# Optimization experiments

Measured on AMD Instinct MI355X. Metric: run time of the kernel, lower is better.

## Reference

```python
import jax, jax.numpy as jnp
import numpy as np

GAMMA = 1.0
EPS = 1e-8


def setup_inputs() -> dict:
    key = jax.random.key(0)
    k1, k2 = jax.random.split(key)
    inputs = jax.random.normal(k1, (16, 2048, 1024), dtype=jnp.float32)
    codebook = jax.random.normal(k2, (2048, 1024), dtype=jnp.float32)  # normal(1.0) init
    return {"inputs": inputs, "codebook": codebook}


def reference(inputs, codebook):
    # inputs: [B, T, D]; codebook: [K, D]
    features = jax.lax.stop_gradient(inputs)
    # similarity = sum over D of features[..., None, :] * codebook -> [B, T, K]
    similarity = jnp.einsum('btd,kd->btk', features, codebook)
    scores = jax.nn.softmax(similarity, axis=-1)  # [B, T, K]
    nn_idx = jnp.argmax(scores, axis=-1)  # [B, T]
    # one_hot(nn_idx) @ codebook == direct gather
    quantized = codebook[nn_idx]  # [B, T, D]
    quantized = quantized - jnp.mean(quantized, axis=-1, keepdims=True)
    quantized = quantized / jnp.linalg.norm(quantized, axis=-1, keepdims=True)
    # entropy loss
    flat = scores.reshape(-1, scores.shape[-1])  # [B*T, K]
    h_clust = -jnp.mean(jnp.sum(flat * jnp.log2(flat + EPS), axis=-1))
    diversity = jnp.mean(flat, axis=0)  # [K]
    h_diversity = -jnp.sum(diversity * jnp.log2(diversity + EPS))
    loss = h_clust - GAMMA * h_diversity
    quantization_loss = jnp.full(scores.shape, loss)  # [B, T, K], scalar broadcast
    # straight-through estimator
    quantized = inputs + jax.lax.stop_gradient(quantized - inputs)
    return (quantized, quantization_loss, nn_idx, codebook)
```

## Files before the change

### kernel.cpp

```cpp
#include <hip/hip_runtime.h>
#include <math.h>

#define M_TOTAL 32768
#define D_DIM   1024
#define K_DIM   2048

#define OUT0_OFF 0ULL
#define OUT1_OFF 33554432ULL
#define OUT2_OFF 100663296ULL
#define OUT3_OFF 100696064ULL

typedef _Float16 f16x4 __attribute__((ext_vector_type(4)));
typedef _Float16 f16x8 __attribute__((ext_vector_type(8)));
typedef float    f32x4 __attribute__((ext_vector_type(4)));

__device__ __forceinline__ void async_copy16(void* lds, const void* g) {
    __builtin_amdgcn_global_load_lds(
        (const __attribute__((address_space(1))) unsigned int*)g,
        (__attribute__((address_space(3))) unsigned int*)lds, 16, 0, 0);
}

__global__ __launch_bounds__(256) void convcb_kernel(const float* __restrict__ C,
                                                     _Float16* __restrict__ ch,
                                                     _Float16* __restrict__ cl) {
    const int i = blockIdx.x * 256 + threadIdx.x;
    const float4 c = ((const float4*)C)[i];
    f16x4 h, l;
    h.x = (_Float16)c.x; l.x = (_Float16)(c.x - (float)h.x);
    h.y = (_Float16)c.y; l.y = (_Float16)(c.y - (float)h.y);
    h.z = (_Float16)c.z; l.z = (_Float16)(c.z - (float)h.z);
    h.w = (_Float16)c.w; l.w = (_Float16)(c.w - (float)h.w);
    ((f16x4*)ch)[i] = h;
    ((f16x4*)cl)[i] = l;
}

__global__ __launch_bounds__(256) void gemm_kernel(const float* __restrict__ X,
                                                   const _Float16* __restrict__ CH,
                                                   const _Float16* __restrict__ CL,
                                                   float* __restrict__ S) {
    __shared__ _Float16 Ah[128 * 32];
    __shared__ _Float16 Bh[128 * 32];
    __shared__ _Float16 Bl[128 * 32];

    const int tid  = threadIdx.x;
    const int lane = tid & 63;
    const int wave = tid >> 6;
    const int n0 = blockIdx.x * 128;
    const int m0 = blockIdx.y * 128;
    const int wm = (wave & 1) * 64;
    const int wn = (wave >> 1) * 64;
    const int fr = lane & 15;
    const int fq = lane >> 4;

    f32x4 acc[4][4];
#pragma unroll
    for (int mi = 0; mi < 4; mi++)
#pragma unroll
        for (int ni = 0; ni < 4; ni++) {
            acc[mi][ni].x = 0.f; acc[mi][ni].y = 0.f;
            acc[mi][ni].z = 0.f; acc[mi][ni].w = 0.f;
        }

    for (int k0 = 0; k0 < D_DIM; k0 += 32) {
#pragma unroll
        for (int e = 0; e < 2; e++) {
            const int u   = wave * 128 + e * 64 + lane;
            const int row = u >> 2;
            const int off = u & 3;
            const size_t gofs = (size_t)(n0 + row) * D_DIM + k0 + off * 8;
            async_copy16((void*)(Bh + (size_t)(wave * 128 + e * 64) * 8), (const void*)(CH + gofs));
            async_copy16((void*)(Bl + (size_t)(wave * 128 + e * 64) * 8), (const void*)(CL + gofs));
        }
#pragma unroll
        for (int i = 0; i < 4; i++) {
            const int f = i * 256 + tid;
            const int r = f >> 3;
            const int q = f & 7;
            const float4 a = *(const float4*)(X + (size_t)(m0 + r) * D_DIM + k0 + q * 4);
            f16x4 h;
            h.x = (_Float16)a.x; h.y = (_Float16)a.y;
            h.z = (_Float16)a.z; h.w = (_Float16)a.w;
            *(f16x4*)(Ah + r * 32 + q * 4) = h;
        }
        __syncthreads();

        f16x8 afrag[4], bhfrag[4], blfrag[4];
#pragma unroll
        for (int t = 0; t < 4; t++) {
            afrag[t]  = *(const f16x8*)(Ah + (wm + t * 16 + fr) * 32 + fq * 8);
            bhfrag[t] = *(const f16x8*)(Bh + (wn + t * 16 + fr) * 32 + fq * 8);
            blfrag[t] = *(const f16x8*)(Bl + (wn + t * 16 + fr) * 32 + fq * 8);
        }
#pragma unroll
        for (int mi = 0; mi < 4; mi++)
#pragma unroll
            for (int ni = 0; ni < 4; ni++) {
                acc[mi][ni] = __builtin_amdgcn_mfma_f32_16x16x32_f16(afrag[mi], bhfrag[ni], acc[mi][ni], 0, 0, 0);
                acc[mi][ni] = __builtin_amdgcn_mfma_f32_16x16x32_f16(afrag[mi], blfrag[ni], acc[mi][ni], 0, 0, 0);
            }
        __syncthreads();
    }

#pragma unroll
    for (int mi = 0; mi < 4; mi++)
#pragma unroll
        for (int r = 0; r < 4; r++) {
            float* dst = S + (size_t)(m0 + wm + mi * 16 + fq * 4 + r) * K_DIM + n0 + wn;
#pragma unroll
            for (int ni = 0; ni < 4; ni++) dst[ni * 16 + fr] = acc[mi][ni][r];
        }
}

#define MARGIN 0.125f
__global__ __launch_bounds__(256) void rowstats_kernel(const float* __restrict__ S,
                                                       int* __restrict__ cnt,
                                                       int* __restrict__ cand,
                                                       float* __restrict__ div_acc,
                                                       float* __restrict__ hclust_acc) {
    __shared__ float sdiv[K_DIM];
    const int tid = threadIdx.x;
    for (int k = tid; k < K_DIM; k += 256) sdiv[k] = 0.0f;
    __syncthreads();

    const int lane = tid & 63;
    const int wave = tid >> 6;

    float dreg[32];
#pragma unroll
    for (int j = 0; j < 32; j++) dreg[j] = 0.0f;
    float ent_acc = 0.0f;

    for (int r8 = 0; r8 < 8; r8++) {
        const int row = blockIdx.x * 32 + wave * 8 + r8;
        const float* srow = S + (size_t)row * K_DIM;

        float v[32];
#pragma unroll
        for (int j = 0; j < 32; j++) v[j] = srow[lane + 64 * j];

        float m = v[0];
#pragma unroll
        for (int j = 1; j < 32; j++) m = fmaxf(m, v[j]);
        for (int off = 32; off > 0; off >>= 1) m = fmaxf(m, __shfl_xor(m, off, 64));

        const float thresh = m - MARGIN;
#pragma unroll
        for (int j = 0; j < 32; j++) {
            if (v[j] > thresh) {
                const int slot = atomicAdd(&cnt[row], 1);
                if (slot < 8) cand[row * 8 + slot] = lane + 64 * j;
            }
        }

        float Z = 0.0f;
#pragma unroll
        for (int j = 0; j < 32; j++) {
            v[j] = __expf(v[j] - m);
            Z += v[j];
        }
        for (int off = 32; off > 0; off >>= 1) Z += __shfl_xor(Z, off, 64);
        const float invZ = 1.0f / Z;

#pragma unroll
        for (int j = 0; j < 32; j++) {
            const float p = v[j] * invZ;
            dreg[j] += p;
            ent_acc += p * __log2f(p + 1e-8f);
        }
    }

#pragma unroll
    for (int j = 0; j < 32; j++) atomicAdd(&sdiv[lane + 64 * j], dreg[j]);
    for (int off = 32; off > 0; off >>= 1) ent_acc += __shfl_xor(ent_acc, off, 64);
    if (lane == 0) atomicAdd(hclust_acc, ent_acc);
    __syncthreads();

    for (int k = tid; k < K_DIM; k += 256) atomicAdd(&div_acc[k], sdiv[k]);
}

__global__ __launch_bounds__(256) void refine_kernel(const float* __restrict__ X,
                                                     const float* __restrict__ C,
                                                     const int* __restrict__ cnt,
                                                     const int* __restrict__ cand,
                                                     float* __restrict__ nn_out) {
    const int tid = threadIdx.x;
    const int lane = tid & 63;
    const int wave = tid >> 6;
    const int row = blockIdx.x * 4 + wave;

    const int n = min(cnt[row], 8);
    const float* x = X + (size_t)row * D_DIM;

    float4 xv[4];
#pragma unroll
    for (int q = 0; q < 4; q++) xv[q] = *(const float4*)(x + lane * 4 + 256 * q);

    double bestv = -1.0e300;
    int besti = 0x7fffffff;
    for (int c = 0; c < n; c++) {
        const int idx = cand[row * 8 + c];
        const float* cb = C + (size_t)idx * D_DIM;
        double s = 0.0;
#pragma unroll
        for (int q = 0; q < 4; q++) {
            const float4 cv = *(const float4*)(cb + lane * 4 + 256 * q);
            s += (double)xv[q].x * cv.x + (double)xv[q].y * cv.y +
                 (double)xv[q].z * cv.z + (double)xv[q].w * cv.w;
        }
        for (int off = 32; off > 0; off >>= 1) s += __shfl_xor(s, off, 64);
        if (s > bestv || (s == bestv && idx < besti)) { bestv = s; besti = idx; }
    }
    if (lane == 0) nn_out[row] = (float)besti;
}

__global__ __launch_bounds__(256) void finalize_kernel(const float* __restrict__ div_acc,
                                                       const float* __restrict__ hclust_acc,
                                                       float* __restrict__ loss_out) {
    __shared__ float red[256];
    const int tid = threadIdx.x;
    float sum = 0.0f;
    for (int k = tid; k < K_DIM; k += 256) {
        const float d = div_acc[k] * (1.0f / 32768.0f);
        sum += d * __log2f(d + 1e-8f);
    }
    red[tid] = sum;
    __syncthreads();
    for (int s = 128; s > 0; s >>= 1) {
        if (tid < s) red[tid] += red[tid + s];
        __syncthreads();
    }
    if (tid == 0) {
        const float h_clust = -hclust_acc[0] * (1.0f / 32768.0f);
        const float h_div = -red[0];
        loss_out[0] = h_clust - 1.0f * h_div;
    }
}

__global__ __launch_bounds__(256) void fill_kernel(float* __restrict__ out1,
                                                   const float* __restrict__ loss_ptr) {
    const float v = loss_ptr[0];
    const float4 f = make_float4(v, v, v, v);
    float4* o = (float4*)out1;
    const size_t stride = (size_t)gridDim.x * blockDim.x;
    for (size_t i = (size_t)blockIdx.x * blockDim.x + threadIdx.x; i < 16777216ULL; i += stride)
        o[i] = f;
}

__global__ __launch_bounds__(256) void quantize_kernel(const float* __restrict__ C,
                                                       const float* __restrict__ nn_f,
                                                       float* __restrict__ out0) {
    const int tid = threadIdx.x;
    const int lane = tid & 63;
    const int wave = tid >> 6;
    const int row = blockIdx.x * 4 + wave;

    const int idx = (int)nn_f[row];
    const float* c = C + (size_t)idx * D_DIM;

    float4 v[4];
    float sum = 0.0f;
#pragma unroll
    for (int q = 0; q < 4; q++) {
        v[q] = *(const float4*)(c + lane * 4 + 256 * q);
        sum += v[q].x + v[q].y + v[q].z + v[q].w;
    }
    for (int off = 32; off > 0; off >>= 1) sum += __shfl_xor(sum, off, 64);
    const float mean = sum * (1.0f / 1024.0f);

    float ss = 0.0f;
#pragma unroll
    for (int q = 0; q < 4; q++) {
        v[q].x -= mean; v[q].y -= mean; v[q].z -= mean; v[q].w -= mean;
        ss += v[q].x * v[q].x + v[q].y * v[q].y + v[q].z * v[q].z + v[q].w * v[q].w;
    }
    for (int off = 32; off > 0; off >>= 1) ss += __shfl_xor(ss, off, 64);
    const float inv = 1.0f / sqrtf(ss);

    float* o = out0 + (size_t)row * D_DIM;
#pragma unroll
    for (int q = 0; q < 4; q++) {
        float4 w = v[q];
        w.x *= inv; w.y *= inv; w.z *= inv; w.w *= inv;
        *(float4*)(o + lane * 4 + 256 * q) = w;
    }
}

__global__ __launch_bounds__(256) void copycb_kernel(const float* __restrict__ C,
                                                     float* __restrict__ out3) {
    const size_t i = (size_t)blockIdx.x * 256 + threadIdx.x;
    if (i < 524288ULL) ((float4*)out3)[i] = ((const float4*)C)[i];
}

extern "C" void kernel_launch(void* const* d_in, const int* in_sizes, int n_in,
                              void* d_out, int out_size, void* d_ws, size_t ws_size,
                              hipStream_t stream) {
    const float* X = (const float*)d_in[0];
    const float* C = (const float*)d_in[1];
    float* out = (float*)d_out;

    char* scratch = (char*)d_out;
    _Float16* CH  = (_Float16*)(scratch);
    _Float16* CL  = (_Float16*)(scratch + (4 << 20));
    int* cand     = (int*)(scratch + (8 << 20));
    int* cnt      = (int*)(scratch + (9 << 20));
    float* div_acc   = (float*)(scratch + (9 << 20) + (128 << 10));
    float* hclust    = div_acc + 2048;
    float* loss      = div_acc + 2049;

    float* S = out + OUT1_OFF;

    hipMemsetAsync(scratch + (9 << 20), 0, (128 << 10) + 8192 + 16, stream);

    convcb_kernel<<<2048, 256, 0, stream>>>(C, CH, CL);

    gemm_kernel<<<dim3(K_DIM / 128, M_TOTAL / 128), 256, 0, stream>>>(X, CH, CL, S);

    rowstats_kernel<<<M_TOTAL / 32, 256, 0, stream>>>(S, cnt, cand, div_acc, hclust);

    refine_kernel<<<M_TOTAL / 4, 256, 0, stream>>>(X, C, cnt, cand, out + OUT2_OFF);

    finalize_kernel<<<1, 256, 0, stream>>>(div_acc, hclust, loss);

    fill_kernel<<<8192, 256, 0, stream>>>(out + OUT1_OFF, loss);

    quantize_kernel<<<M_TOTAL / 4, 256, 0, stream>>>(C, out + OUT2_OFF, out + OUT0_OFF);

    copycb_kernel<<<2048, 256, 0, stream>>>(C, out + OUT3_OFF);
}
```

Baseline: 1.050 ms.

## Pre-convert inputs to fp16, async-load A tiles with XOR-swizzled LDS, fuse codebook copy

Adds a separate pass that converts X to fp16 in scratch. The GEMM can then stage A tiles through global_load_lds async copies, as it already does for B, instead of synchronous float4 loads followed by in-kernel conversion. An XOR swizzle on the 16-byte slot index is applied in both the global-source addressing and the fragment reads to reduce LDS bank conflicts. The codebook output copy is folded into the codebook conversion kernel, which drops one launch. The trade-off is an extra full pass over X (read fp32, write fp16) in exchange for halving the A-operand bytes and the conversion work inside the GEMM.

```diff
diff --git a/kernel.cpp b/kernel.cpp
--- a/kernel.cpp
+++ b/kernel.cpp
@@ -22,7 +22,8 @@
 
 __global__ __launch_bounds__(256) void convcb_kernel(const float* __restrict__ C,
                                                      _Float16* __restrict__ ch,
-                                                     _Float16* __restrict__ cl) {
+                                                     _Float16* __restrict__ cl,
+                                                     float* __restrict__ out3) {
     const int i = blockIdx.x * 256 + threadIdx.x;
     const float4 c = ((const float4*)C)[i];
     f16x4 h, l;
@@ -32,9 +33,20 @@
     h.w = (_Float16)c.w; l.w = (_Float16)(c.w - (float)h.w);
     ((f16x4*)ch)[i] = h;
     ((f16x4*)cl)[i] = l;
-}
-
-__global__ __launch_bounds__(256) void gemm_kernel(const float* __restrict__ X,
+    ((float4*)out3)[i] = c;
+}
+
+__global__ __launch_bounds__(256) void convx_kernel(const float* __restrict__ X,
+                                                    _Float16* __restrict__ xh) {
+    const size_t i = (size_t)blockIdx.x * 256 + threadIdx.x;
+    const float4 a = ((const float4*)X)[i];
+    f16x4 h;
+    h.x = (_Float16)a.x; h.y = (_Float16)a.y;
+    h.z = (_Float16)a.z; h.w = (_Float16)a.w;
+    ((f16x4*)xh)[i] = h;
+}
+
+__global__ __launch_bounds__(256) void gemm_kernel(const _Float16* __restrict__ XH,
                                                    const _Float16* __restrict__ CH,
                                                    const _Float16* __restrict__ CL,
                                                    float* __restrict__ S) {
@@ -51,6 +63,7 @@
     const int wn = (wave >> 1) * 64;
     const int fr = lane & 15;
     const int fq = lane >> 4;
+    const int fsw = (fr >> 1) & 3;
 
     f32x4 acc[4][4];
 #pragma unroll
@@ -66,30 +79,23 @@
         for (int e = 0; e < 2; e++) {
             const int u   = wave * 128 + e * 64 + lane;
             const int row = u >> 2;
-            const int off = u & 3;
-            const size_t gofs = (size_t)(n0 + row) * D_DIM + k0 + off * 8;
-            async_copy16((void*)(Bh + (size_t)(wave * 128 + e * 64) * 8), (const void*)(CH + gofs));
-            async_copy16((void*)(Bl + (size_t)(wave * 128 + e * 64) * 8), (const void*)(CL + gofs));
-        }
-#pragma unroll
-        for (int i = 0; i < 4; i++) {
-            const int f = i * 256 + tid;
-            const int r = f >> 3;
-            const int q = f & 7;
-            const float4 a = *(const float4*)(X + (size_t)(m0 + r) * D_DIM + k0 + q * 4);
-            f16x4 h;
-            h.x = (_Float16)a.x; h.y = (_Float16)a.y;
-            h.z = (_Float16)a.z; h.w = (_Float16)a.w;
-            *(f16x4*)(Ah + r * 32 + q * 4) = h;
+            const int gslot = (u & 3) ^ ((row >> 1) & 3);
+            const size_t bofs = (size_t)(n0 + row) * D_DIM + k0 + gslot * 8;
+            const size_t aofs = (size_t)(m0 + row) * D_DIM + k0 + gslot * 8;
+            const size_t lofs = (size_t)(wave * 128 + e * 64) * 8;
+            async_copy16((void*)(Ah + lofs), (const void*)(XH + aofs));
+            async_copy16((void*)(Bh + lofs), (const void*)(CH + bofs));
+            async_copy16((void*)(Bl + lofs), (const void*)(CL + bofs));
         }
         __syncthreads();
 
         f16x8 afrag[4], bhfrag[4], blfrag[4];
+        const int sa = (fq ^ fsw) * 8;
 #pragma unroll
         for (int t = 0; t < 4; t++) {
-            afrag[t]  = *(const f16x8*)(Ah + (wm + t * 16 + fr) * 32 + fq * 8);
-            bhfrag[t] = *(const f16x8*)(Bh + (wn + t * 16 + fr) * 32 + fq * 8);
-            blfrag[t] = *(const f16x8*)(Bl + (wn + t * 16 + fr) * 32 + fq * 8);
+            afrag[t]  = *(const f16x8*)(Ah + (wm + t * 16 + fr) * 32 + sa);
+            bhfrag[t] = *(const f16x8*)(Bh + (wn + t * 16 + fr) * 32 + sa);
+            blfrag[t] = *(const f16x8*)(Bl + (wn + t * 16 + fr) * 32 + sa);
         }
 #pragma unroll
         for (int mi = 0; mi < 4; mi++)
@@ -285,12 +291,6 @@
     }
 }
 
-__global__ __launch_bounds__(256) void copycb_kernel(const float* __restrict__ C,
-                                                     float* __restrict__ out3) {
-    const size_t i = (size_t)blockIdx.x * 256 + threadIdx.x;
-    if (i < 524288ULL) ((float4*)out3)[i] = ((const float4*)C)[i];
-}
-
 extern "C" void kernel_launch(void* const* d_in, const int* in_sizes, int n_in,
                               void* d_out, int out_size, void* d_ws, size_t ws_size,
                               hipStream_t stream) {
@@ -306,14 +306,17 @@
     float* div_acc   = (float*)(scratch + (9 << 20) + (128 << 10));
     float* hclust    = div_acc + 2048;
     float* loss      = div_acc + 2049;
+    _Float16* XH  = (_Float16*)(scratch + (16 << 20));
 
     float* S = out + OUT1_OFF;
 
     hipMemsetAsync(scratch + (9 << 20), 0, (128 << 10) + 8192 + 16, stream);
 
-    convcb_kernel<<<2048, 256, 0, stream>>>(C, CH, CL);
-
-    gemm_kernel<<<dim3(K_DIM / 128, M_TOTAL / 128), 256, 0, stream>>>(X, CH, CL, S);
+    convcb_kernel<<<2048, 256, 0, stream>>>(C, CH, CL, out + OUT3_OFF);
+
+    convx_kernel<<<32768, 256, 0, stream>>>(X, XH);
+
+    gemm_kernel<<<dim3(K_DIM / 128, M_TOTAL / 128), 256, 0, stream>>>(XH, CH, CL, S);
 
     rowstats_kernel<<<M_TOTAL / 32, 256, 0, stream>>>(S, cnt, cand, div_acc, hclust);
 
@@ -324,6 +327,4 @@
     fill_kernel<<<8192, 256, 0, stream>>>(out + OUT1_OFF, loss);
 
     quantize_kernel<<<M_TOTAL / 4, 256, 0, stream>>>(C, out + OUT2_OFF, out + OUT0_OFF);
-
-    copycb_kernel<<<2048, 256, 0, stream>>>(C, out + OUT3_OFF);
-}
+}
```

Result: faster. 962.1 us (-8.4%).
